# Performance work log

Hardware: AMD Instinct MI355X
Metric: run time of the kernel (lower is better)

Reference implementation:

```python
import jax, jax.numpy as jnp
import numpy as np
from jax import lax

DIM = 128
K = 3
PAD = K // 2


def setup_inputs() -> dict:
    key = jax.random.key(0)
    k1, k2, k3, k4, k5 = jax.random.split(key, 5)
    B, H, W = 64, 32, 32
    wdim = DIM * DIM * K * K + DIM  # 147584
    # scale question_rep (it encodes conv weights) for numerical sanity
    question_rep = jax.random.normal(k1, (B, wdim), dtype=jnp.float32) * 0.05
    lhs_rep = jax.random.normal(k2, (B, DIM, H, W), dtype=jnp.float32)
    rhs_rep = jax.random.normal(k3, (B, DIM, H, W), dtype=jnp.float32)
    proj_w = jax.random.normal(k4, (DIM, 2 * DIM), dtype=jnp.float32) * (1.0 / np.sqrt(2 * DIM))
    proj_b = jax.random.normal(k5, (DIM,), dtype=jnp.float32) * 0.01
    return {"question_rep": question_rep, "lhs_rep": lhs_rep,
            "rhs_rep": rhs_rep, "proj_w": proj_w, "proj_b": proj_b}


def _per_sample_conv(x, w, b):
    # x: [dim, H, W], w: [dim, dim, K, K], b: [dim]
    y = lax.conv_general_dilated(
        x[None], w, window_strides=(1, 1),
        padding=[(PAD, PAD), (PAD, PAD)],
        dimension_numbers=("NCHW", "OIHW", "NCHW"))
    return y[0] + b[:, None, None]


def reference(question_rep, lhs_rep, rhs_rep, proj_w, proj_b):
    B = question_rep.shape[0]
    wdim = DIM * DIM * K * K
    cnn_weight = question_rep[:, :wdim].reshape(B, DIM, DIM, K, K)
    cnn_bias = question_rep[:, wdim:]  # [B, dim]
    # 1x1 projection conv: cat along channels then contract
    cat = jnp.concatenate([lhs_rep, rhs_rep], axis=1)  # [B, 2*dim, H, W]
    cnn_inp = jnp.einsum("bchw,oc->bohw", cat, proj_w) + proj_b[None, :, None, None]
    # per-sample dynamic conv, vectorized over batch (equiv. grouped conv)
    out = jax.vmap(_per_sample_conv)(cnn_inp, cnn_weight, cnn_bias)
    return out
```

## Files before the change

kernel.cpp:

```cpp
#include <hip/hip_runtime.h>
#include <hip/hip_bf16.h>

#define QSTRIDE 147584
#define WOFF    147456

typedef __attribute__((ext_vector_type(8))) short bf16x8;
typedef __attribute__((ext_vector_type(4))) float f32x4;

static __device__ __forceinline__ ushort f2bf(float f) {
  union { float f; unsigned u; } x; x.f = f;
  unsigned r = x.u + 0x7fffu + ((x.u >> 16) & 1u);
  return (ushort)(r >> 16);
}
static __device__ __forceinline__ unsigned pk2(ushort a, ushort b) {
  return (unsigned)a | ((unsigned)b << 16);
}
static __device__ __forceinline__ void async16(const ushort* g, ushort* l) {
  __builtin_amdgcn_global_load_lds((const __attribute__((address_space(1))) void*)g,
                                   (__attribute__((address_space(3))) void*)l, 16, 0, 0);
}

__global__ __launch_bounds__(256) void pack_w_kernel(const float* __restrict__ q,
                                                     ushort* __restrict__ wt2) {
  __shared__ float Ls[4608];
  int b = blockIdx.x >> 3, ogrp = blockIdx.x & 7;
  int t = threadIdx.x;
  const float* gbase = q + (size_t)b * QSTRIDE + (size_t)ogrp * 16 * 1152;
  ushort* dstb = wt2 + (size_t)b * 147456;
  int o_loc = t >> 6;
  int ci    = (t & 63) * 2;
  int cq    = ci >> 5, coff = ci & 31;
  for (int r = 0; r < 4; ++r) {
    __syncthreads();
    const float* gs = gbase + r * 4608;
#pragma unroll
    for (int i = 0; i < 18; ++i) Ls[i * 256 + t] = gs[i * 256 + t];
    __syncthreads();
    int o_full = ogrp * 16 + r * 4 + o_loc;
    const float* v = Ls + o_loc * 1152 + ci * 9;
    float a[18];
#pragma unroll
    for (int i = 0; i < 18; ++i) a[i] = v[i];
    ushort* dd = dstb + (size_t)cq * 4096 + o_full * 32 + coff;
#pragma unroll
    for (int tap = 0; tap < 9; ++tap) {
      unsigned pkv = pk2(f2bf(a[tap]), f2bf(a[9 + tap]));
      *(unsigned*)(dd + (size_t)tap * 16384) = pkv;
    }
  }
}

__global__ __launch_bounds__(256) void pack_pw_kernel(const float* __restrict__ pw,
                                                      ushort* __restrict__ pwb2) {
  int tg = blockIdx.x * 256 + threadIdx.x;
  int o  = tg >> 5;
  int c0 = (tg & 31) * 8;
  const float4* s4 = (const float4*)(pw + (size_t)o * 256 + c0);
  float4 f0 = s4[0], f1 = s4[1];
  uint4 pkv;
  pkv.x = pk2(f2bf(f0.x), f2bf(f0.y)); pkv.y = pk2(f2bf(f0.z), f2bf(f0.w));
  pkv.z = pk2(f2bf(f1.x), f2bf(f1.y)); pkv.w = pk2(f2bf(f1.z), f2bf(f1.w));
  *(uint4*)(pwb2 + (size_t)(c0 >> 5) * 4096 + o * 32 + (c0 & 31)) = pkv;
}

__global__ __launch_bounds__(256) void zero_border_kernel(ushort* __restrict__ xp2) {
  int b = blockIdx.x, t = threadIdx.x;
  for (int idx = t; idx < 528; idx += 256) {
    int cq = idx / 132, r = idx - cq * 132;
    int hp, wp;
    if (r < 34)       { hp = 0;        wp = r; }
    else if (r < 68)  { hp = 33;       wp = r - 34; }
    else if (r < 100) { hp = r - 67;   wp = 0; }
    else              { hp = r - 99;   wp = 33; }
    uint4 z = {0u,0u,0u,0u};
    uint4* dst = (uint4*)(xp2 + (((size_t)b * 4 + cq) * 1156 + hp * 34 + wp) * 32);
#pragma unroll
    for (int i = 0; i < 4; ++i) dst[i] = z;
  }
}

__global__ __launch_bounds__(256, 2) void proj_kernel(const ushort* __restrict__ pwb2,
                                                      const float* __restrict__ lhs,
                                                      const float* __restrict__ rhs,
                                                      const float* __restrict__ pb,
                                                      ushort* __restrict__ xp2) {
  __shared__ ushort As[128 * 32];
  __shared__ ushort Bs[128 * 32];
  int b = blockIdx.y, tile = blockIdx.x;
  int p0 = tile * 128;
  int t = threadIdx.x;
  int lane = t & 63, wv = t >> 6;
  int m0 = (wv & 1) * 64, n0 = (wv >> 1) * 64;
  int quad = lane >> 4, li = lane & 15;
  f32x4 acc[4][4] = {};
  int cgrp = t & 3;
  int pq   = t >> 2;

  for (int c0 = 0; c0 < 256; c0 += 32) {
    const float* src = (c0 < 128 ? lhs : rhs) + (size_t)b * 131072
                     + (size_t)((c0 & 127) + cgrp * 8) * 1024 + p0 + 2 * pq;
    ushort u0[8], u1[8];
#pragma unroll
    for (int j = 0; j < 8; ++j) {
      float2 f = *(const float2*)(src + (size_t)j * 1024);
      u0[j] = f2bf(f.x); u1[j] = f2bf(f.y);
    }
    __syncthreads();
    {
      const ushort* ag = pwb2 + (size_t)(c0 >> 5) * 4096;
      async16(ag + (size_t)wv * 512 + lane * 8,       As + wv * 512);
      async16(ag + (size_t)(wv + 4) * 512 + lane * 8, As + (wv + 4) * 512);
    }
    {
      uint4 pk0, pk1;
      pk0.x = pk2(u0[0],u0[1]); pk0.y = pk2(u0[2],u0[3]);
      pk0.z = pk2(u0[4],u0[5]); pk0.w = pk2(u0[6],u0[7]);
      pk1.x = pk2(u1[0],u1[1]); pk1.y = pk2(u1[2],u1[3]);
      pk1.z = pk2(u1[4],u1[5]); pk1.w = pk2(u1[6],u1[7]);
      *(uint4*)(Bs + (size_t)(2*pq)   * 32 + cgrp * 8) = pk0;
      *(uint4*)(Bs + (size_t)(2*pq+1) * 32 + cgrp * 8) = pk1;
    }
    __syncthreads();
    bf16x8 af[4], bg[4];
#pragma unroll
    for (int mi = 0; mi < 4; ++mi)
      af[mi] = *(const bf16x8*)(As + (m0 + mi*16 + li) * 32 + quad * 8);
#pragma unroll
    for (int ni = 0; ni < 4; ++ni)
      bg[ni] = *(const bf16x8*)(Bs + (n0 + ni*16 + li) * 32 + quad * 8);
#pragma unroll
    for (int mi = 0; mi < 4; ++mi)
#pragma unroll
      for (int ni = 0; ni < 4; ++ni)
        acc[mi][ni] = __builtin_amdgcn_mfma_f32_16x16x32_bf16(af[mi], bg[ni], acc[mi][ni], 0, 0, 0);
  }

  ushort* xpb = xp2 + (size_t)b * 4 * 1156 * 32;
#pragma unroll
  for (int mi = 0; mi < 4; ++mi) {
    int o0 = m0 + mi*16 + quad*4;
    float4 bias = *(const float4*)(pb + o0);
#pragma unroll
    for (int ni = 0; ni < 4; ++ni) {
      int p = p0 + n0 + ni*16 + li;
      int h = p >> 5, w = p & 31;
      ushort* dp = xpb + ((size_t)(o0 >> 5) * 1156 + (h + 1) * 34 + (w + 1)) * 32 + (o0 & 31);
      f32x4 a = acc[mi][ni];
      uint2 pkv;
      pkv.x = pk2(f2bf(a.x + bias.x), f2bf(a.y + bias.y));
      pkv.y = pk2(f2bf(a.z + bias.z), f2bf(a.w + bias.w));
      *(uint2*)dp = pkv;
    }
  }
}

__global__ __launch_bounds__(256, 2) void conv_kernel(const ushort* __restrict__ wt2,
                                                      const ushort* __restrict__ xp2,
                                                      const float* __restrict__ q,
                                                      float* __restrict__ out) {
  __shared__ ushort As[2][4096];
  __shared__ ushort Bs[6528];
  int blk = blockIdx.x;
  int b = blk & 63, tile = blk >> 6;
  int p0 = tile * 128, h0 = tile * 4;
  int t = threadIdx.x;
  int lane = t & 63, wv = t >> 6;
  int m0 = (wv & 1) * 64, n0 = (wv >> 1) * 64;
  int quad = lane >> 4, li = lane & 15;
  f32x4 acc[4][4] = {};
  const ushort* wtb = wt2 + (size_t)b * 147456;
  const ushort* xpb = xp2 + (size_t)b * 147968;

  for (int cq = 0; cq < 4; ++cq) {
    __syncthreads();
    {
      const ushort* bgp = xpb + (size_t)(cq * 1156 + h0 * 34) * 32;
#pragma unroll
      for (int p = 0; p < 3; ++p)
        async16(bgp + (size_t)(p * 256 + t) * 8, Bs + p * 2048 + wv * 512);
      if (t < 48)
        async16(bgp + (size_t)(768 + t) * 8, Bs + 6144);
    }
    {
      const ushort* ag = wtb + (size_t)cq * 4096;
      async16(ag + (size_t)t * 8,         As[0] + wv * 512);
      async16(ag + (size_t)(256 + t) * 8, As[0] + 2048 + wv * 512);
    }
    for (int tap = 0; tap < 9; ++tap) {
      __syncthreads();
      if (tap < 8) {
        const ushort* ag = wtb + (size_t)((tap + 1) * 4 + cq) * 4096;
        ushort* ab = As[(tap + 1) & 1];
        async16(ag + (size_t)t * 8,         ab + wv * 512);
        async16(ag + (size_t)(256 + t) * 8, ab + 2048 + wv * 512);
      }
      int kh = tap / 3, kw = tap - kh * 3;
      const ushort* ar = As[tap & 1];
      bf16x8 af[4], bg[4];
#pragma unroll
      for (int mi = 0; mi < 4; ++mi)
        af[mi] = *(const bf16x8*)(ar + (m0 + mi*16 + li) * 32 + quad * 8);
#pragma unroll
      for (int ni = 0; ni < 4; ++ni) {
        int pl = n0 + ni*16 + li;
        int h = pl >> 5, w = pl & 31;
        bg[ni] = *(const bf16x8*)(Bs + ((h + kh) * 34 + (w + kw)) * 32 + quad * 8);
      }
#pragma unroll
      for (int mi = 0; mi < 4; ++mi)
#pragma unroll
        for (int ni = 0; ni < 4; ++ni)
          acc[mi][ni] = __builtin_amdgcn_mfma_f32_16x16x32_bf16(af[mi], bg[ni], acc[mi][ni], 0, 0, 0);
    }
  }

  const float* qb = q + (size_t)b * QSTRIDE + WOFF;
  float* ob = out + (size_t)b * 128 * 1024 + p0;
#pragma unroll
  for (int mi = 0; mi < 4; ++mi) {
    int o0 = m0 + mi*16 + quad*4;
    float4 bias = *(const float4*)(qb + o0);
#pragma unroll
    for (int ni = 0; ni < 4; ++ni) {
      int pl = n0 + ni*16 + li;
      float* dp = ob + (size_t)o0 * 1024 + pl;
      f32x4 a = acc[mi][ni];
      dp[0]    = a.x + bias.x;
      dp[1024] = a.y + bias.y;
      dp[2048] = a.z + bias.z;
      dp[3072] = a.w + bias.w;
    }
  }
}

extern "C" void kernel_launch(void* const* d_in, const int* in_sizes, int n_in,
                              void* d_out, int out_size, void* d_ws, size_t ws_size,
                              hipStream_t stream) {
  const float* q   = (const float*)d_in[0];
  const float* lhs = (const float*)d_in[1];
  const float* rhs = (const float*)d_in[2];
  const float* pw  = (const float*)d_in[3];
  const float* pb  = (const float*)d_in[4];
  float* out = (float*)d_out;

  char* ws = (char*)d_ws;
  ushort* wt2  = (ushort*)(ws);
  ushort* pwb2 = (ushort*)(ws + 18874368);
  ushort* xp2  = (ushort*)(ws + 18939904);

  pack_w_kernel     <<<512, 256, 0, stream>>>(q, wt2);
  pack_pw_kernel    <<<16,  256, 0, stream>>>(pw, pwb2);
  zero_border_kernel<<<64,  256, 0, stream>>>(xp2);
  proj_kernel       <<<dim3(8, 64), 256, 0, stream>>>(pwb2, lhs, rhs, pb, xp2);
  conv_kernel       <<<512, 256, 0, stream>>>(wt2, xp2, q, out);
}
```

Measured before the change: 182.2 us.

## Drop LDS staging in weight pack, projection, and conv weight operands

The weight-pack kernel now reads float4 vectors straight from global memory, with no shared-memory transpose, over twice as many blocks. The projection kernel loses its shared-memory tiles: each wave loads its activations and the projection weights directly into registers and feeds 8 MFMAs per chunk, on smaller 64-pixel tiles with higher occupancy. The conv kernel reads the per-sample weight fragments straight from global/L2 instead of double-buffering them through LDS, and instead double-buffers the input halo tile across channel groups. This removes many barriers and LDS round-trips, at the cost of uncoalesced, cache-dependent global weight reads inside the MFMA loop.

```diff
diff --git a/kernel.cpp b/kernel.cpp
--- a/kernel.cpp
+++ b/kernel.cpp
@@ -22,31 +22,24 @@
 
 __global__ __launch_bounds__(256) void pack_w_kernel(const float* __restrict__ q,
                                                      ushort* __restrict__ wt2) {
-  __shared__ float Ls[4608];
-  int b = blockIdx.x >> 3, ogrp = blockIdx.x & 7;
+  int b = blockIdx.x >> 4, og = blockIdx.x & 15;
   int t = threadIdx.x;
-  const float* gbase = q + (size_t)b * QSTRIDE + (size_t)ogrp * 16 * 1152;
-  ushort* dstb = wt2 + (size_t)b * 147456;
-  int o_loc = t >> 6;
-  int ci    = (t & 63) * 2;
-  int cq    = ci >> 5, coff = ci & 31;
-  for (int r = 0; r < 4; ++r) {
-    __syncthreads();
-    const float* gs = gbase + r * 4608;
-#pragma unroll
-    for (int i = 0; i < 18; ++i) Ls[i * 256 + t] = gs[i * 256 + t];
-    __syncthreads();
-    int o_full = ogrp * 16 + r * 4 + o_loc;
-    const float* v = Ls + o_loc * 1152 + ci * 9;
-    float a[18];
-#pragma unroll
-    for (int i = 0; i < 18; ++i) a[i] = v[i];
-    ushort* dd = dstb + (size_t)cq * 4096 + o_full * 32 + coff;
-#pragma unroll
-    for (int tap = 0; tap < 9; ++tap) {
-      unsigned pkv = pk2(f2bf(a[tap]), f2bf(a[9 + tap]));
-      *(unsigned*)(dd + (size_t)tap * 16384) = pkv;
-    }
+  int o_loc = t >> 5, cq = (t >> 3) & 3, q4 = t & 7;
+  int o_full = og * 8 + o_loc;
+  int ci = cq * 32 + q4 * 4;
+  const float4* src = (const float4*)(q + (size_t)b * QSTRIDE
+                                        + (size_t)o_full * 1152 + (size_t)ci * 9);
+  float4 ff[9];
+#pragma unroll
+  for (int i = 0; i < 9; ++i) ff[i] = src[i];
+  const float* v = (const float*)ff;
+  ushort* dd = wt2 + (size_t)b * 147456 + (size_t)cq * 4096 + o_full * 32 + q4 * 4;
+#pragma unroll
+  for (int tap = 0; tap < 9; ++tap) {
+    uint2 pkv;
+    pkv.x = pk2(f2bf(v[tap]),      f2bf(v[9 + tap]));
+    pkv.y = pk2(f2bf(v[18 + tap]), f2bf(v[27 + tap]));
+    *(uint2*)(dd + (size_t)tap * 16384) = pkv;
   }
 }
 
@@ -79,78 +72,52 @@
   }
 }
 
-__global__ __launch_bounds__(256, 2) void proj_kernel(const ushort* __restrict__ pwb2,
+__global__ __launch_bounds__(256, 4) void proj_kernel(const ushort* __restrict__ pwb2,
                                                       const float* __restrict__ lhs,
                                                       const float* __restrict__ rhs,
                                                       const float* __restrict__ pb,
                                                       ushort* __restrict__ xp2) {
-  __shared__ ushort As[128 * 32];
-  __shared__ ushort Bs[128 * 32];
-  int b = blockIdx.y, tile = blockIdx.x;
-  int p0 = tile * 128;
+  int b = blockIdx.y, p0 = blockIdx.x * 64;
   int t = threadIdx.x;
   int lane = t & 63, wv = t >> 6;
-  int m0 = (wv & 1) * 64, n0 = (wv >> 1) * 64;
   int quad = lane >> 4, li = lane & 15;
-  f32x4 acc[4][4] = {};
-  int cgrp = t & 3;
-  int pq   = t >> 2;
-
-  for (int c0 = 0; c0 < 256; c0 += 32) {
-    const float* src = (c0 < 128 ? lhs : rhs) + (size_t)b * 131072
-                     + (size_t)((c0 & 127) + cgrp * 8) * 1024 + p0 + 2 * pq;
-    ushort u0[8], u1[8];
-#pragma unroll
-    for (int j = 0; j < 8; ++j) {
-      float2 f = *(const float2*)(src + (size_t)j * 1024);
-      u0[j] = f2bf(f.x); u1[j] = f2bf(f.y);
+  int px = p0 + wv * 16 + li;
+  f32x4 acc[8] = {};
+  const float* bl = lhs + (size_t)b * 131072 + (size_t)quad * 8192 + px;
+  const float* br = rhs + (size_t)b * 131072 + (size_t)quad * 8192 + px;
+
+#pragma unroll
+  for (int c = 0; c < 8; ++c) {
+    const float* s = (c < 4 ? bl : br) + (size_t)(c & 3) * 32768;
+    float f[8];
+#pragma unroll
+    for (int j = 0; j < 8; ++j) f[j] = s[(size_t)j * 1024];
+    union { uint4 u; bf16x8 v; } bu;
+    bu.u.x = pk2(f2bf(f[0]), f2bf(f[1]));
+    bu.u.y = pk2(f2bf(f[2]), f2bf(f[3]));
+    bu.u.z = pk2(f2bf(f[4]), f2bf(f[5]));
+    bu.u.w = pk2(f2bf(f[6]), f2bf(f[7]));
+    bf16x8 bg = bu.v;
+    const ushort* ap = pwb2 + (size_t)c * 4096 + li * 32 + quad * 8;
+#pragma unroll
+    for (int mi = 0; mi < 8; ++mi) {
+      bf16x8 af = *(const bf16x8*)(ap + mi * 512);
+      acc[mi] = __builtin_amdgcn_mfma_f32_16x16x32_bf16(af, bg, acc[mi], 0, 0, 0);
     }
-    __syncthreads();
-    {
-      const ushort* ag = pwb2 + (size_t)(c0 >> 5) * 4096;
-      async16(ag + (size_t)wv * 512 + lane * 8,       As + wv * 512);
-      async16(ag + (size_t)(wv + 4) * 512 + lane * 8, As + (wv + 4) * 512);
-    }
-    {
-      uint4 pk0, pk1;
-      pk0.x = pk2(u0[0],u0[1]); pk0.y = pk2(u0[2],u0[3]);
-      pk0.z = pk2(u0[4],u0[5]); pk0.w = pk2(u0[6],u0[7]);
-      pk1.x = pk2(u1[0],u1[1]); pk1.y = pk2(u1[2],u1[3]);
-      pk1.z = pk2(u1[4],u1[5]); pk1.w = pk2(u1[6],u1[7]);
-      *(uint4*)(Bs + (size_t)(2*pq)   * 32 + cgrp * 8) = pk0;
-      *(uint4*)(Bs + (size_t)(2*pq+1) * 32 + cgrp * 8) = pk1;
-    }
-    __syncthreads();
-    bf16x8 af[4], bg[4];
-#pragma unroll
-    for (int mi = 0; mi < 4; ++mi)
-      af[mi] = *(const bf16x8*)(As + (m0 + mi*16 + li) * 32 + quad * 8);
-#pragma unroll
-    for (int ni = 0; ni < 4; ++ni)
-      bg[ni] = *(const bf16x8*)(Bs + (n0 + ni*16 + li) * 32 + quad * 8);
-#pragma unroll
-    for (int mi = 0; mi < 4; ++mi)
-#pragma unroll
-      for (int ni = 0; ni < 4; ++ni)
-        acc[mi][ni] = __builtin_amdgcn_mfma_f32_16x16x32_bf16(af[mi], bg[ni], acc[mi][ni], 0, 0, 0);
   }
 
   ushort* xpb = xp2 + (size_t)b * 4 * 1156 * 32;
-#pragma unroll
-  for (int mi = 0; mi < 4; ++mi) {
-    int o0 = m0 + mi*16 + quad*4;
+  int h = px >> 5, w = px & 31;
+#pragma unroll
+  for (int mi = 0; mi < 8; ++mi) {
+    int o0 = mi * 16 + quad * 4;
     float4 bias = *(const float4*)(pb + o0);
-#pragma unroll
-    for (int ni = 0; ni < 4; ++ni) {
-      int p = p0 + n0 + ni*16 + li;
-      int h = p >> 5, w = p & 31;
-      ushort* dp = xpb + ((size_t)(o0 >> 5) * 1156 + (h + 1) * 34 + (w + 1)) * 32 + (o0 & 31);
-      f32x4 a = acc[mi][ni];
-      uint2 pkv;
-      pkv.x = pk2(f2bf(a.x + bias.x), f2bf(a.y + bias.y));
-      pkv.y = pk2(f2bf(a.z + bias.z), f2bf(a.w + bias.w));
-      *(uint2*)dp = pkv;
-    }
+    f32x4 a = acc[mi];
+    uint2 pkv;
+    pkv.x = pk2(f2bf(a.x + bias.x), f2bf(a.y + bias.y));
+    pkv.y = pk2(f2bf(a.z + bias.z), f2bf(a.w + bias.w));
+    ushort* dp = xpb + ((size_t)(o0 >> 5) * 1156 + (h + 1) * 34 + (w + 1)) * 32 + (o0 & 31);
+    *(uint2*)dp = pkv;
   }
 }
 
@@ -158,8 +125,7 @@
                                                       const ushort* __restrict__ xp2,
                                                       const float* __restrict__ q,
                                                       float* __restrict__ out) {
-  __shared__ ushort As[2][4096];
-  __shared__ ushort Bs[6528];
+  __shared__ ushort Bs[2][6528];
   int blk = blockIdx.x;
   int b = blk & 63, tile = blk >> 6;
   int p0 = tile * 128, h0 = tile * 4;
@@ -171,31 +137,28 @@
   const ushort* wtb = wt2 + (size_t)b * 147456;
   const ushort* xpb = xp2 + (size_t)b * 147968;
 
+  auto stageB = [&](int cqi, int buf) {
+    const ushort* bgp = xpb + (size_t)(cqi * 1156 + h0 * 34) * 32;
+    int lb = wv * 204;
+    async16(bgp + (size_t)(lb +       lane) * 8, &Bs[buf][0] + (lb      ) * 8);
+    async16(bgp + (size_t)(lb +  64 + lane) * 8, &Bs[buf][0] + (lb +  64) * 8);
+    async16(bgp + (size_t)(lb + 128 + lane) * 8, &Bs[buf][0] + (lb + 128) * 8);
+    if (lane < 12)
+      async16(bgp + (size_t)(lb + 192 + lane) * 8, &Bs[buf][0] + (lb + 192) * 8);
+  };
+
+  stageB(0, 0);
+
+#pragma unroll
   for (int cq = 0; cq < 4; ++cq) {
     __syncthreads();
-    {
-      const ushort* bgp = xpb + (size_t)(cq * 1156 + h0 * 34) * 32;
-#pragma unroll
-      for (int p = 0; p < 3; ++p)
-        async16(bgp + (size_t)(p * 256 + t) * 8, Bs + p * 2048 + wv * 512);
-      if (t < 48)
-        async16(bgp + (size_t)(768 + t) * 8, Bs + 6144);
-    }
-    {
-      const ushort* ag = wtb + (size_t)cq * 4096;
-      async16(ag + (size_t)t * 8,         As[0] + wv * 512);
-      async16(ag + (size_t)(256 + t) * 8, As[0] + 2048 + wv * 512);
-    }
+    if (cq < 3) stageB(cq + 1, (cq + 1) & 1);
+    const ushort* bsr = &Bs[cq & 1][0];
+    const ushort* wcq = wtb + (size_t)cq * 4096;
+#pragma unroll
     for (int tap = 0; tap < 9; ++tap) {
-      __syncthreads();
-      if (tap < 8) {
-        const ushort* ag = wtb + (size_t)((tap + 1) * 4 + cq) * 4096;
-        ushort* ab = As[(tap + 1) & 1];
-        async16(ag + (size_t)t * 8,         ab + wv * 512);
-        async16(ag + (size_t)(256 + t) * 8, ab + 2048 + wv * 512);
-      }
+      const ushort* ar = wcq + (size_t)tap * 16384;
       int kh = tap / 3, kw = tap - kh * 3;
-      const ushort* ar = As[tap & 1];
       bf16x8 af[4], bg[4];
 #pragma unroll
       for (int mi = 0; mi < 4; ++mi)
@@ -203,8 +166,8 @@
 #pragma unroll
       for (int ni = 0; ni < 4; ++ni) {
         int pl = n0 + ni*16 + li;
-        int h = pl >> 5, w = pl & 31;
-        bg[ni] = *(const bf16x8*)(Bs + ((h + kh) * 34 + (w + kw)) * 32 + quad * 8);
+        int hh = pl >> 5, ww = pl & 31;
+        bg[ni] = *(const bf16x8*)(bsr + ((hh + kh) * 34 + (ww + kw)) * 32 + quad * 8);
       }
 #pragma unroll
       for (int mi = 0; mi < 4; ++mi)
@@ -248,9 +211,9 @@
   ushort* pwb2 = (ushort*)(ws + 18874368);
   ushort* xp2  = (ushort*)(ws + 18939904);
 
-  pack_w_kernel     <<<512, 256, 0, stream>>>(q, wt2);
-  pack_pw_kernel    <<<16,  256, 0, stream>>>(pw, pwb2);
-  zero_border_kernel<<<64,  256, 0, stream>>>(xp2);
-  proj_kernel       <<<dim3(8, 64), 256, 0, stream>>>(pwb2, lhs, rhs, pb, xp2);
-  conv_kernel       <<<512, 256, 0, stream>>>(wt2, xp2, q, out);
-}
+  pack_w_kernel     <<<1024, 256, 0, stream>>>(q, wt2);
+  pack_pw_kernel    <<<16,   256, 0, stream>>>(pw, pwb2);
+  zero_border_kernel<<<64,   256, 0, stream>>>(xp2);
+  proj_kernel       <<<dim3(16, 64), 256, 0, stream>>>(pwb2, lhs, rhs, pb, xp2);
+  conv_kernel       <<<512,  256, 0, stream>>>(wt2, xp2, q, out);
+}
```

Result: slower. 193.9 us (+6.4%).
